# Optimization experiments

Measured on AMD Instinct MI355X. Metric: run time of the kernel, lower is better.

The kernel has to match this reference:

```python
import jax, jax.numpy as jnp
import numpy as np

D_MODEL = 1024
D_HIDDEN = 4096
N_EXPERTS = 8
B, S = 2, 2048


def setup_inputs() -> dict:
    key = jax.random.key(0)
    ks = jax.random.split(key, 4)
    sd = 1.0 / np.sqrt(D_MODEL)
    sh = 1.0 / np.sqrt(D_HIDDEN)
    return {
        "x": jax.random.normal(ks[0], (B, S, D_MODEL), dtype=jnp.float32),
        "Wg": jax.random.normal(ks[1], (D_MODEL, N_EXPERTS), dtype=jnp.float32) * sd,
        "bg": jnp.zeros((N_EXPERTS,), dtype=jnp.float32),
        "W1": jax.random.normal(ks[2], (N_EXPERTS, D_MODEL, D_HIDDEN), dtype=jnp.float32) * sd,
        "b1": jnp.zeros((N_EXPERTS, D_HIDDEN), dtype=jnp.float32),
        "W2": jax.random.normal(ks[3], (N_EXPERTS, D_HIDDEN, D_MODEL), dtype=jnp.float32) * sh,
        "b2": jnp.zeros((N_EXPERTS, D_MODEL), dtype=jnp.float32),
    }


def reference(x, Wg, bg, W1, b1, W2, b2):
    # Router: softmax is monotone, so argmax(softmax(logits)) == argmax(logits).
    logits = jnp.einsum("bsd,de->bse", x, Wg) + bg
    expert_idx = jnp.argmax(logits, axis=-1)  # [B, S]
    # Top-1 dispatch, expressed as compute-all-experts + per-token select
    # (jit-friendly; the torch loop masks/gathers per expert).
    h = jax.nn.gelu(jnp.einsum("bsd,edh->bseh", x, W1) + b1, approximate=False)
    y = jnp.einsum("bseh,ehd->bsed", h, W2) + b2  # [B, S, E, D]
    out = jnp.take_along_axis(y, expert_idx[:, :, None, None], axis=2)[:, :, 0, :]
    return out
```

## Files before the change

### kernel.cpp

```cpp
#include <hip/hip_runtime.h>
#include <hip/hip_bf16.h>
#include <math.h>

#define D_MODEL 1024
#define D_HIDDEN 4096
#define N_EXP 8
#define N_TOK 4096

typedef __attribute__((ext_vector_type(8))) __bf16 bf16x8_t;
typedef __attribute__((ext_vector_type(4))) float f32x4_t;

#define WS_BUCKET_OFF 256
#define WS_XB_OFF     ((size_t)1 << 18)
#define WS_H_OFF      (((size_t)1 << 18) + ((size_t)8 << 20))
#define WS_W1B_OFF    (((size_t)1 << 18) + ((size_t)40 << 20))
#define WS_W2B_OFF    (((size_t)1 << 18) + ((size_t)104 << 20))
#define WS_NEED       (((size_t)1 << 18) + ((size_t)168 << 20))

__device__ __forceinline__ void gload16(const void* g, void* l) {
    __builtin_amdgcn_global_load_lds(
        (__attribute__((address_space(1))) void*)(g),
        (__attribute__((address_space(3))) void*)(l),
        16, 0, 0);
}

__global__ __launch_bounds__(64) void init_counts(int* counts) {
    if (threadIdx.x < N_EXP) counts[threadIdx.x] = 0;
}

__global__ __launch_bounds__(256) void router_kernel(
    const float* __restrict__ x, const float* __restrict__ Wg,
    const float* __restrict__ bg, int* __restrict__ counts,
    int* __restrict__ bucket, __hip_bfloat16* __restrict__ xb)
{
    const int wid  = threadIdx.x >> 6;
    const int lane = threadIdx.x & 63;
    const int t    = blockIdx.x * 4 + wid;
    const float* xr = x + (size_t)t * D_MODEL;

    double acc[N_EXP];
#pragma unroll
    for (int e = 0; e < N_EXP; ++e) acc[e] = 0.0;

#pragma unroll
    for (int j = 0; j < D_MODEL / 64; ++j) {
        const int d = j * 64 + lane;
        const float xv = xr[d];
        xb[(size_t)t * D_MODEL + d] = __float2bfloat16(xv);
        const float4* wr = (const float4*)(Wg + (size_t)d * N_EXP);
        const float4 w0 = wr[0], w1 = wr[1];
        const double xd = (double)xv;
        acc[0] += xd * (double)w0.x; acc[1] += xd * (double)w0.y;
        acc[2] += xd * (double)w0.z; acc[3] += xd * (double)w0.w;
        acc[4] += xd * (double)w1.x; acc[5] += xd * (double)w1.y;
        acc[6] += xd * (double)w1.z; acc[7] += xd * (double)w1.w;
    }
#pragma unroll
    for (int e = 0; e < N_EXP; ++e) {
        double v = acc[e];
#pragma unroll
        for (int off = 32; off >= 1; off >>= 1) v += __shfl_xor(v, off, 64);
        acc[e] = v + (double)bg[e];
    }
    if (lane == 0) {
        int best = 0; double bv = acc[0];
#pragma unroll
        for (int e = 1; e < N_EXP; ++e)
            if (acc[e] > bv) { bv = acc[e]; best = e; }
        const int pos = atomicAdd(&counts[best], 1);
        bucket[best * N_TOK + pos] = t;
    }
}

template<int KT, int NT>
__global__ __launch_bounds__(256) void convert_w(
    const float* __restrict__ W, __hip_bfloat16* __restrict__ Wb)
{
    const int e  = blockIdx.z;
    const int k0 = blockIdx.y * 64;
    const int n0 = blockIdx.x * 64;
    const int tid = threadIdx.x;
    const int w   = tid >> 6;
    const int lane = tid & 63;

    __shared__ __hip_bfloat16 Lt[64 * 68];

    const float* src = W + (size_t)e * KT * NT + (size_t)k0 * NT + n0 + lane;
#pragma unroll
    for (int r = 0; r < 4; ++r) {
        const int kk = w * 16 + r * 4;
        union { __hip_bfloat16 hh[4]; unsigned long long u; } pk;
#pragma unroll
        for (int s = 0; s < 4; ++s)
            pk.hh[s] = __float2bfloat16(src[(size_t)(kk + s) * NT]);
        *(unsigned long long*)((char*)Lt + (size_t)lane * 136 + kk * 2) = pk.u;
    }
    __syncthreads();

    const int nr   = w * 16 + (lane >> 2);
    const int half = lane & 3;
    const char* rp = (const char*)Lt + (size_t)nr * 136 + half * 32;
    const uint2 a0 = *(const uint2*)(rp);
    const uint2 a1 = *(const uint2*)(rp + 8);
    const uint2 b0 = *(const uint2*)(rp + 16);
    const uint2 b1 = *(const uint2*)(rp + 24);
    __hip_bfloat16* op = Wb + (size_t)e * NT * KT + (size_t)(n0 + nr) * KT + k0 + half * 16;
    *(uint4*)op       = make_uint4(a0.x, a0.y, a1.x, a1.y);
    *(uint4*)(op + 8) = make_uint4(b0.x, b0.y, b1.x, b1.y);
}

template<int K_TOT, int N_TOT, int BN, bool IS_FFN1>
__global__ __launch_bounds__(256, 2) void ffn_gemm_bf16(
    const __hip_bfloat16* __restrict__ A,
    const __hip_bfloat16* __restrict__ Wb,
    const float* __restrict__ bias,
    const int* __restrict__ counts,
    const int* __restrict__ bucket,
    __hip_bfloat16* __restrict__ hout,
    float* __restrict__ yout)
{
    constexpr int NG  = BN / 32;
    constexpr int NBI = BN / 32;

    const int e   = blockIdx.z;
    const int cnt = counts[e];
    const int m0  = blockIdx.y * 128;
    if (m0 >= cnt) return;
    const int n0   = blockIdx.x * BN;
    const int tid  = threadIdx.x;
    const int lane = tid & 63;
    const int wid  = tid >> 6;
    const int wm   = wid >> 1, wn = wid & 1;

    __shared__ __hip_bfloat16 As[128 * 64];
    __shared__ __hip_bfloat16 Bs[BN * 64];
    __shared__ int s_tok[128];

    if (tid < 128) {
        int idx = m0 + tid;
        if (idx >= cnt) idx = cnt - 1;
        s_tok[tid] = bucket[e * N_TOK + idx];
    }
    __syncthreads();

    const __hip_bfloat16* gA[4]; char* lA[4];
#pragma unroll
    for (int i = 0; i < 4; ++i) {
        const int r = wid * 32 + i * 8 + (lane >> 3);
        gA[i] = A + (size_t)s_tok[r] * K_TOT + (((lane & 7) ^ (r & 7)) << 3);
        lA[i] = (char*)As + (size_t)(wid * 32 + i * 8) * 128;
    }
    const __hip_bfloat16* gB[NBI]; char* lB[NBI];
    const __hip_bfloat16* wbase = Wb + (size_t)e * N_TOT * K_TOT;
#pragma unroll
    for (int i = 0; i < NBI; ++i) {
        const int r = wid * (BN / 4) + i * 8 + (lane >> 3);
        gB[i] = wbase + (size_t)(n0 + r) * K_TOT + (((lane & 7) ^ (r & 7)) << 3);
        lB[i] = (char*)Bs + (size_t)(wid * (BN / 4) + i * 8) * 128;
    }

    f32x4_t acc[4][NG];
#pragma unroll
    for (int f = 0; f < 4; ++f)
#pragma unroll
        for (int g = 0; g < NG; ++g) acc[f][g] = (f32x4_t){0.f, 0.f, 0.f, 0.f};

    for (int k0 = 0; k0 < K_TOT; k0 += 64) {
#pragma unroll
        for (int i = 0; i < 4; ++i) gload16(gA[i] + k0, lA[i]);
#pragma unroll
        for (int i = 0; i < NBI; ++i) gload16(gB[i] + k0, lB[i]);
        __syncthreads();

#pragma unroll
        for (int kk = 0; kk < 2; ++kk) {
            uint4 af[4], bf[NG];
            const int ko = kk * 4 + (lane >> 4);
#pragma unroll
            for (int f = 0; f < 4; ++f) {
                const int r = wm * 64 + f * 16 + (lane & 15);
                af[f] = *(const uint4*)((const char*)As + r * 128 + ((ko ^ (r & 7)) << 4));
            }
#pragma unroll
            for (int g = 0; g < NG; ++g) {
                const int n = wn * (BN / 2) + g * 16 + (lane & 15);
                bf[g] = *(const uint4*)((const char*)Bs + n * 128 + ((ko ^ (n & 7)) << 4));
            }
#pragma unroll
            for (int f = 0; f < 4; ++f)
#pragma unroll
                for (int g = 0; g < NG; ++g)
                    acc[f][g] = __builtin_amdgcn_mfma_f32_16x16x32_bf16(
                        __builtin_bit_cast(bf16x8_t, af[f]),
                        __builtin_bit_cast(bf16x8_t, bf[g]),
                        acc[f][g], 0, 0, 0);
        }
        __syncthreads();
    }

#pragma unroll
    for (int f = 0; f < 4; ++f) {
#pragma unroll
        for (int j = 0; j < 4; ++j) {
            const int rl = wm * 64 + f * 16 + (lane >> 4) * 4 + j;
            const bool ok = (m0 + rl) < cnt;
            const int tok = s_tok[rl];
#pragma unroll
            for (int g = 0; g < NG; ++g) {
                const int col = n0 + wn * (BN / 2) + g * 16 + (lane & 15);
                float v = acc[f][g][j] + bias[e * N_TOT + col];
                if (IS_FFN1) {
                    v = 0.5f * v * (1.0f + erff(v * 0.70710678118654752f));
                    if (ok) hout[(size_t)tok * N_TOT + col] = __float2bfloat16(v);
                } else {
                    if (ok) yout[(size_t)tok * N_TOT + col] = v;
                }
            }
        }
    }
}

template<int K_TOT, int N_TOT, bool IS_FFN1>
__global__ __launch_bounds__(256, 2) void ffn_gemm_f32(
    const __hip_bfloat16* __restrict__ A,
    const float* __restrict__ W,
    const float* __restrict__ bias,
    const int* __restrict__ counts,
    const int* __restrict__ bucket,
    __hip_bfloat16* __restrict__ hout,
    float* __restrict__ yout)
{
    const int e   = blockIdx.z;
    const int cnt = counts[e];
    const int m0  = blockIdx.y * 128;
    if (m0 >= cnt) return;
    const int n0   = blockIdx.x * 128;
    const int tid  = threadIdx.x;
    const int lane = tid & 63;
    const int wid  = tid >> 6;
    const int wm   = wid >> 1, wn = wid & 1;

    __shared__ __hip_bfloat16 As[128 * 64];
    __shared__ __hip_bfloat16 Bs[128 * 64];
    __shared__ int s_tok[128];

    if (tid < 128) {
        int idx = m0 + tid;
        if (idx >= cnt) idx = cnt - 1;
        s_tok[tid] = bucket[e * N_TOK + idx];
    }
    __syncthreads();

    const __hip_bfloat16* gA[4]; char* lA[4];
#pragma unroll
    for (int i = 0; i < 4; ++i) {
        const int r = wid * 32 + i * 8 + (lane >> 3);
        gA[i] = A + (size_t)s_tok[r] * K_TOT + (((lane & 7) ^ (r & 7)) << 3);
        lA[i] = (char*)As + (size_t)(wid * 32 + i * 8) * 128;
    }
    const int ko_t = lane & 7;
    const int nq   = wid * 8 + (lane >> 3);
    const float* wb = W + (size_t)e * K_TOT * N_TOT + (size_t)(ko_t * 8) * N_TOT + n0 + nq * 4;

    f32x4_t acc[4][4];
#pragma unroll
    for (int f = 0; f < 4; ++f)
#pragma unroll
        for (int g = 0; g < 4; ++g) acc[f][g] = (f32x4_t){0.f, 0.f, 0.f, 0.f};

    for (int k0 = 0; k0 < K_TOT; k0 += 64) {
#pragma unroll
        for (int i = 0; i < 4; ++i) gload16(gA[i] + k0, lA[i]);
        const float* wk = wb + (size_t)k0 * N_TOT;
        float4 v[8];
#pragma unroll
        for (int j = 0; j < 8; ++j) v[j] = *(const float4*)(wk + (size_t)j * N_TOT);
#pragma unroll
        for (int i = 0; i < 4; ++i) {
            const int n = nq * 4 + i;
            union { __hip_bfloat16 hh[8]; uint4 u; } pk;
#pragma unroll
            for (int j = 0; j < 8; ++j) pk.hh[j] = __float2bfloat16(((const float*)&v[j])[i]);
            *(uint4*)((char*)Bs + n * 128 + ((ko_t ^ (n & 7)) << 4)) = pk.u;
        }
        __syncthreads();

#pragma unroll
        for (int kk = 0; kk < 2; ++kk) {
            uint4 af[4], bf[4];
            const int ko = kk * 4 + (lane >> 4);
#pragma unroll
            for (int f = 0; f < 4; ++f) {
                const int r = wm * 64 + f * 16 + (lane & 15);
                af[f] = *(const uint4*)((const char*)As + r * 128 + ((ko ^ (r & 7)) << 4));
            }
#pragma unroll
            for (int g = 0; g < 4; ++g) {
                const int n = wn * 64 + g * 16 + (lane & 15);
                bf[g] = *(const uint4*)((const char*)Bs + n * 128 + ((ko ^ (n & 7)) << 4));
            }
#pragma unroll
            for (int f = 0; f < 4; ++f)
#pragma unroll
                for (int g = 0; g < 4; ++g)
                    acc[f][g] = __builtin_amdgcn_mfma_f32_16x16x32_bf16(
                        __builtin_bit_cast(bf16x8_t, af[f]),
                        __builtin_bit_cast(bf16x8_t, bf[g]),
                        acc[f][g], 0, 0, 0);
        }
        __syncthreads();
    }

#pragma unroll
    for (int f = 0; f < 4; ++f) {
#pragma unroll
        for (int j = 0; j < 4; ++j) {
            const int rl = wm * 64 + f * 16 + (lane >> 4) * 4 + j;
            const bool ok = (m0 + rl) < cnt;
            const int tok = s_tok[rl];
#pragma unroll
            for (int g = 0; g < 4; ++g) {
                const int col = n0 + wn * 64 + g * 16 + (lane & 15);
                float v = acc[f][g][j] + bias[e * N_TOT + col];
                if (IS_FFN1) {
                    v = 0.5f * v * (1.0f + erff(v * 0.70710678118654752f));
                    if (ok) hout[(size_t)tok * N_TOT + col] = __float2bfloat16(v);
                } else {
                    if (ok) yout[(size_t)tok * N_TOT + col] = v;
                }
            }
        }
    }
}

extern "C" void kernel_launch(void* const* d_in, const int* in_sizes, int n_in,
                              void* d_out, int out_size, void* d_ws, size_t ws_size,
                              hipStream_t stream) {
    const float* x  = (const float*)d_in[0];
    const float* Wg = (const float*)d_in[1];
    const float* bg = (const float*)d_in[2];
    const float* W1 = (const float*)d_in[3];
    const float* b1 = (const float*)d_in[4];
    const float* W2 = (const float*)d_in[5];
    const float* b2 = (const float*)d_in[6];
    float* out = (float*)d_out;

    char* ws = (char*)d_ws;
    int* counts = (int*)(ws);
    int* bucket = (int*)(ws + WS_BUCKET_OFF);
    __hip_bfloat16* xb  = (__hip_bfloat16*)(ws + WS_XB_OFF);
    __hip_bfloat16* h   = (__hip_bfloat16*)(ws + WS_H_OFF);
    __hip_bfloat16* w1b = (__hip_bfloat16*)(ws + WS_W1B_OFF);
    __hip_bfloat16* w2b = (__hip_bfloat16*)(ws + WS_W2B_OFF);

    init_counts<<<dim3(1), dim3(64), 0, stream>>>(counts);
    router_kernel<<<dim3(N_TOK / 4), dim3(256), 0, stream>>>(x, Wg, bg, counts, bucket, xb);

    if (ws_size >= WS_NEED) {
        convert_w<D_MODEL, D_HIDDEN><<<dim3(D_HIDDEN / 64, D_MODEL / 64, N_EXP), dim3(256), 0, stream>>>(W1, w1b);
        convert_w<D_HIDDEN, D_MODEL><<<dim3(D_MODEL / 64, D_HIDDEN / 64, N_EXP), dim3(256), 0, stream>>>(W2, w2b);
        ffn_gemm_bf16<D_MODEL, D_HIDDEN, 128, true>
            <<<dim3(D_HIDDEN / 128, N_TOK / 128, N_EXP), dim3(256), 0, stream>>>(
                xb, w1b, b1, counts, bucket, h, nullptr);
        ffn_gemm_bf16<D_HIDDEN, D_MODEL, 64, false>
            <<<dim3(D_MODEL / 64, N_TOK / 128, N_EXP), dim3(256), 0, stream>>>(
                h, w2b, b2, counts, bucket, nullptr, out);
    } else {
        ffn_gemm_f32<D_MODEL, D_HIDDEN, true>
            <<<dim3(D_HIDDEN / 128, N_TOK / 128, N_EXP), dim3(256), 0, stream>>>(
                xb, W1, b1, counts, bucket, h, nullptr);
        ffn_gemm_f32<D_HIDDEN, D_MODEL, false>
            <<<dim3(D_MODEL / 128, N_TOK / 128, N_EXP), dim3(256), 0, stream>>>(
                h, W2, b2, counts, bucket, nullptr, out);
    }
}
```

Baseline: 315.6 us.

## Double-buffer GEMM LDS tiles, remap grid for XCD locality, vectorize weight conversion

The bf16 GEMM now double-buffers the A/B LDS tiles, issuing the next K-tile's async global->LDS loads before computing on the current tile, so memory latency overlaps MFMA work. It also flattens the grid to 1D and remaps block IDs round-robin across 8 groups so an expert's tiles stay together on one XCD for L2 reuse, and raises minimum occupancy for FFN2. The weight bf16 conversion kernel switches to float4 coalesced loads. Doubled LDS use may reduce occupancy. Many blocks still exit early because a full grid is launched for each expert, so the remap changes which blocks sit idle.

```diff
diff --git a/kernel.cpp b/kernel.cpp
--- a/kernel.cpp
+++ b/kernel.cpp
@@ -80,23 +80,29 @@
     const int k0 = blockIdx.y * 64;
     const int n0 = blockIdx.x * 64;
     const int tid = threadIdx.x;
-    const int w   = tid >> 6;
+
+    __shared__ __hip_bfloat16 Lt[64 * 68];
+
+    const int q  = tid & 15;
+    const int kb = tid >> 4;
+    const float* src = W + (size_t)e * KT * NT + (size_t)(k0 + kb * 4) * NT + n0 + q * 4;
+    float4 v0 = *(const float4*)(src);
+    float4 v1 = *(const float4*)(src + (size_t)NT);
+    float4 v2 = *(const float4*)(src + (size_t)2 * NT);
+    float4 v3 = *(const float4*)(src + (size_t)3 * NT);
+#pragma unroll
+    for (int i = 0; i < 4; ++i) {
+        union { __hip_bfloat16 hh[4]; unsigned long long u; } pk;
+        pk.hh[0] = __float2bfloat16(((const float*)&v0)[i]);
+        pk.hh[1] = __float2bfloat16(((const float*)&v1)[i]);
+        pk.hh[2] = __float2bfloat16(((const float*)&v2)[i]);
+        pk.hh[3] = __float2bfloat16(((const float*)&v3)[i]);
+        *(unsigned long long*)((char*)Lt + (size_t)(q * 4 + i) * 136 + kb * 8) = pk.u;
+    }
+    __syncthreads();
+
+    const int w    = tid >> 6;
     const int lane = tid & 63;
-
-    __shared__ __hip_bfloat16 Lt[64 * 68];
-
-    const float* src = W + (size_t)e * KT * NT + (size_t)k0 * NT + n0 + lane;
-#pragma unroll
-    for (int r = 0; r < 4; ++r) {
-        const int kk = w * 16 + r * 4;
-        union { __hip_bfloat16 hh[4]; unsigned long long u; } pk;
-#pragma unroll
-        for (int s = 0; s < 4; ++s)
-            pk.hh[s] = __float2bfloat16(src[(size_t)(kk + s) * NT]);
-        *(unsigned long long*)((char*)Lt + (size_t)lane * 136 + kk * 2) = pk.u;
-    }
-    __syncthreads();
-
     const int nr   = w * 16 + (lane >> 2);
     const int half = lane & 3;
     const char* rp = (const char*)Lt + (size_t)nr * 136 + half * 32;
@@ -109,8 +115,8 @@
     *(uint4*)(op + 8) = make_uint4(b0.x, b0.y, b1.x, b1.y);
 }
 
-template<int K_TOT, int N_TOT, int BN, bool IS_FFN1>
-__global__ __launch_bounds__(256, 2) void ffn_gemm_bf16(
+template<int K_TOT, int N_TOT, int BN, int MINW, bool IS_FFN1>
+__global__ __launch_bounds__(256, MINW) void ffn_gemm_bf16(
     const __hip_bfloat16* __restrict__ A,
     const __hip_bfloat16* __restrict__ Wb,
     const float* __restrict__ bias,
@@ -121,19 +127,29 @@
 {
     constexpr int NG  = BN / 32;
     constexpr int NBI = BN / 32;
-
-    const int e   = blockIdx.z;
+    constexpr int NB  = N_TOT / BN;
+    constexpr int MB  = N_TOK / 128;
+    constexpr int NWG = NB * MB * N_EXP;
+    constexpr int ASZ = 128 * 64 * 2;
+    constexpr int BSZ = BN * 64 * 2;
+    constexpr int NT  = K_TOT / 64;
+
+    const int orig = blockIdx.x;
+    const int wg   = (orig & 7) * (NWG >> 3) + (orig >> 3);
+    const int e    = wg / (NB * MB);
+    const int rem  = wg % (NB * MB);
+    const int n0   = (rem / MB) * BN;
+    const int m0   = (rem % MB) * 128;
+
     const int cnt = counts[e];
-    const int m0  = blockIdx.y * 128;
     if (m0 >= cnt) return;
-    const int n0   = blockIdx.x * BN;
     const int tid  = threadIdx.x;
     const int lane = tid & 63;
     const int wid  = tid >> 6;
     const int wm   = wid >> 1, wn = wid & 1;
 
-    __shared__ __hip_bfloat16 As[128 * 64];
-    __shared__ __hip_bfloat16 Bs[BN * 64];
+    __shared__ __hip_bfloat16 As[2 * 128 * 64];
+    __shared__ __hip_bfloat16 Bs[2 * BN * 64];
     __shared__ int s_tok[128];
 
     if (tid < 128) {
@@ -165,13 +181,24 @@
 #pragma unroll
         for (int g = 0; g < NG; ++g) acc[f][g] = (f32x4_t){0.f, 0.f, 0.f, 0.f};
 
-    for (int k0 = 0; k0 < K_TOT; k0 += 64) {
-#pragma unroll
-        for (int i = 0; i < 4; ++i) gload16(gA[i] + k0, lA[i]);
-#pragma unroll
-        for (int i = 0; i < NBI; ++i) gload16(gB[i] + k0, lB[i]);
-        __syncthreads();
-
+#pragma unroll
+    for (int i = 0; i < 4; ++i) gload16(gA[i], lA[i]);
+#pragma unroll
+    for (int i = 0; i < NBI; ++i) gload16(gB[i], lB[i]);
+    __syncthreads();
+
+    int cur = 0;
+    for (int t = 0; t < NT; ++t) {
+        if (t + 1 < NT) {
+            const int k1 = (t + 1) * 64;
+            const int nb = (cur ^ 1);
+#pragma unroll
+            for (int i = 0; i < 4; ++i) gload16(gA[i] + k1, lA[i] + nb * ASZ);
+#pragma unroll
+            for (int i = 0; i < NBI; ++i) gload16(gB[i] + k1, lB[i] + nb * BSZ);
+        }
+        const char* asb = (const char*)As + cur * ASZ;
+        const char* bsb = (const char*)Bs + cur * BSZ;
 #pragma unroll
         for (int kk = 0; kk < 2; ++kk) {
             uint4 af[4], bf[NG];
@@ -179,12 +206,12 @@
 #pragma unroll
             for (int f = 0; f < 4; ++f) {
                 const int r = wm * 64 + f * 16 + (lane & 15);
-                af[f] = *(const uint4*)((const char*)As + r * 128 + ((ko ^ (r & 7)) << 4));
+                af[f] = *(const uint4*)(asb + r * 128 + ((ko ^ (r & 7)) << 4));
             }
 #pragma unroll
             for (int g = 0; g < NG; ++g) {
                 const int n = wn * (BN / 2) + g * 16 + (lane & 15);
-                bf[g] = *(const uint4*)((const char*)Bs + n * 128 + ((ko ^ (n & 7)) << 4));
+                bf[g] = *(const uint4*)(bsb + n * 128 + ((ko ^ (n & 7)) << 4));
             }
 #pragma unroll
             for (int f = 0; f < 4; ++f)
@@ -196,6 +223,7 @@
                         acc[f][g], 0, 0, 0);
         }
         __syncthreads();
+        cur ^= 1;
     }
 
 #pragma unroll
@@ -359,11 +387,11 @@
     if (ws_size >= WS_NEED) {
         convert_w<D_MODEL, D_HIDDEN><<<dim3(D_HIDDEN / 64, D_MODEL / 64, N_EXP), dim3(256), 0, stream>>>(W1, w1b);
         convert_w<D_HIDDEN, D_MODEL><<<dim3(D_MODEL / 64, D_HIDDEN / 64, N_EXP), dim3(256), 0, stream>>>(W2, w2b);
-        ffn_gemm_bf16<D_MODEL, D_HIDDEN, 128, true>
-            <<<dim3(D_HIDDEN / 128, N_TOK / 128, N_EXP), dim3(256), 0, stream>>>(
+        ffn_gemm_bf16<D_MODEL, D_HIDDEN, 128, 2, true>
+            <<<dim3((D_HIDDEN / 128) * (N_TOK / 128) * N_EXP), dim3(256), 0, stream>>>(
                 xb, w1b, b1, counts, bucket, h, nullptr);
-        ffn_gemm_bf16<D_HIDDEN, D_MODEL, 64, false>
-            <<<dim3(D_MODEL / 64, N_TOK / 128, N_EXP), dim3(256), 0, stream>>>(
+        ffn_gemm_bf16<D_HIDDEN, D_MODEL, 64, 3, false>
+            <<<dim3((D_MODEL / 64) * (N_TOK / 128) * N_EXP), dim3(256), 0, stream>>>(
                 h, w2b, b2, counts, bucket, nullptr, out);
     } else {
         ffn_gemm_f32<D_MODEL, D_HIDDEN, true>
```

New measurement: 387.3 us. +22.7%, slower.
